# Kernel optimization log

Hardware: AMD Instinct MI355X
Metric: run time of the kernel (lower is better)

## Reference

```python
import jax, jax.numpy as jnp
import numpy as np

N_QUESTIONS = 2000
N_CATS = 4
MEMORY_SIZE = 50
KEY_DIM = 50
VALUE_DIM = 200
FINAL_FC = 50
ABILITY_SCALE = 3.0
BATCH = 1024
SEQ_LEN = 500


def setup_inputs() -> dict:
    key = jax.random.key(0)
    ks = jax.random.split(key, 20)
    f32 = jnp.float32
    inp = {}
    # integer data: question ids in [1, n_questions], responses in [0, K)
    inp['q_data'] = jax.random.randint(ks[0], (BATCH, SEQ_LEN), 1, N_QUESTIONS + 1)
    inp['r_data'] = jax.random.randint(ks[1], (BATCH, SEQ_LEN), 0, N_CATS)
    s = 0.05
    inp['q_embed_w'] = jax.random.normal(ks[2], (N_QUESTIONS + 1, KEY_DIM), f32) * s
    inp['Mk'] = jax.random.normal(ks[3], (MEMORY_SIZE, KEY_DIM), f32) * s
    inp['Mv0'] = jax.random.normal(ks[4], (MEMORY_SIZE, VALUE_DIM), f32) * s
    inp['Wv'] = jax.random.normal(ks[5], (VALUE_DIM, N_CATS * N_QUESTIONS), f32) * s
    inp['bv'] = jnp.zeros((VALUE_DIM,), f32)
    # DKVMN erase / add transforms
    inp['We'] = jax.random.normal(ks[6], (VALUE_DIM, VALUE_DIM), f32) * s
    inp['be'] = jnp.zeros((VALUE_DIM,), f32)
    inp['Wa'] = jax.random.normal(ks[7], (VALUE_DIM, VALUE_DIM), f32) * s
    inp['ba'] = jnp.zeros((VALUE_DIM,), f32)
    # summary network
    inp['Ws'] = jax.random.normal(ks[8], (FINAL_FC, VALUE_DIM + KEY_DIM), f32) * s
    inp['bs'] = jnp.zeros((FINAL_FC,), f32)
    # ability / threshold / discrimination heads
    inp['Wth'] = jax.random.normal(ks[9], (1, FINAL_FC), f32) * s
    inp['bth'] = jnp.zeros((1,), f32)
    inp['Wbeta'] = jax.random.normal(ks[10], (N_CATS - 1, KEY_DIM), f32) * s
    inp['bbeta'] = jnp.zeros((N_CATS - 1,), f32)
    inp['Wdisc'] = jax.random.normal(ks[11], (1, FINAL_FC + KEY_DIM), f32) * s
    inp['bdisc'] = jnp.zeros((1,), f32)
    return inp


def _deep_gpcm(q_data, r_data, q_embed_w, Mk, Mv0, Wv, bv, We, be, Wa, ba,
               Ws, bs, Wth, bth, Wbeta, bbeta, Wdisc, bdisc):
    B, S = q_data.shape
    K = Wbeta.shape[0] + 1
    D = Wv.shape[0]
    Q = Wv.shape[1] // K
    # view gpcm_value_embed weight as (D, K, Q): one-hot(q) @ W == gather column q
    WvK = Wv.reshape(D, K, Q)
    k_idx = jnp.arange(K, dtype=jnp.float32)
    Mv_init = jnp.broadcast_to(Mv0[None], (B,) + Mv0.shape)

    def step(Mv, inp):
        q_t, r_t = inp  # (B,), (B,)
        qe = q_embed_w[q_t]  # (B, key_dim)
        # linear decay weights: max(0, 1 - |k - r| / (K-1))
        w = jnp.maximum(0.0, 1.0 - jnp.abs(k_idx[None, :] - r_t[:, None].astype(jnp.float32)) / (K - 1))  # (B, K)
        Wvq = jnp.take(WvK, q_t - 1, axis=2)  # (D, K, B)
        ve = jnp.einsum('dkb,bk->bd', Wvq, w) + bv  # value embedding (B, D)
        # DKVMN attention + read
        cw = jax.nn.softmax(qe @ Mk.T, axis=-1)  # (B, mem)
        read = jnp.einsum('bm,bmd->bd', cw, Mv)
        # summary / IRT heads
        summary = jnp.tanh(jnp.concatenate([read, qe], axis=-1) @ Ws.T + bs)  # (B, fc)
        theta = ABILITY_SCALE * (summary @ Wth.T + bth)[:, 0]  # (B,)
        betas = jnp.tanh(qe @ Wbeta.T + bbeta)  # (B, K-1)
        alpha = jax.nn.softplus(jnp.concatenate([summary, qe], axis=-1) @ Wdisc.T + bdisc)[:, 0]  # (B,)
        # erase-add memory write
        erase = jax.nn.sigmoid(ve @ We.T + be)
        add = jnp.tanh(ve @ Wa.T + ba)
        Mv_new = Mv * (1.0 - cw[:, :, None] * erase[:, None, :]) + cw[:, :, None] * add[:, None, :]
        # GPCM cumulative logits -> softmax
        cum = jnp.cumsum(alpha[:, None] * (theta[:, None] - betas), axis=-1)  # (B, K-1)
        logits = jnp.concatenate([jnp.zeros((B, 1), cum.dtype), cum], axis=-1)  # (B, K)
        probs = jax.nn.softmax(logits, axis=-1)
        return Mv_new, probs

    _, probs = jax.lax.scan(step, Mv_init, (q_data.T, r_data.T))  # (S, B, K)
    return jnp.transpose(probs, (1, 0, 2))  # (B, S, K)


def reference(q_data, r_data, q_embed_w, Mk, Mv0, Wv, bv, We, be, Wa, ba,
              Ws, bs, Wth, bth, Wbeta, bbeta, Wdisc, bdisc):
    return _deep_gpcm(q_data, r_data, q_embed_w, Mk, Mv0, Wv, bv, We, be, Wa, ba,
                      Ws, bs, Wth, bth, Wbeta, bbeta, Wdisc, bdisc)
```

## Files before the change

kernel.cpp:

```cpp
#include <hip/hip_runtime.h>
#include <hip/hip_bf16.h>
#include <cstdint>
#include <cstddef>


namespace {
constexpr int kB   = 1024;
constexpr int kS   = 500;
constexpr int kQ   = 2000;
constexpr int kKD  = 50;
constexpr int kMem = 50;
constexpr int kD   = 200;
constexpr int kFC  = 50;
constexpr int kWP  = 216;

constexpr size_t OFF_EAD  = 0;
constexpr size_t OFF_CW   = OFF_EAD + (size_t)kQ * 4 * kD * 2;
constexpr size_t OFF_SQ   = OFF_CW + 100064;
constexpr size_t OFF_BQ   = OFF_SQ + 100064;
constexpr size_t OFF_DQ   = OFF_BQ + 8032;
constexpr size_t OFF_CE   = OFF_DQ + 2016;
constexpr size_t OFF_CA   = OFF_CE + 224;
constexpr size_t OFF_WET  = OFF_CA + 224;
constexpr size_t OFF_WAT  = OFF_WET + 40000;
}

typedef float f32x2 __attribute__((ext_vector_type(2)));
typedef _Float16 h2_t __attribute__((ext_vector_type(2)));

__device__ __forceinline__ f32x2 pk_fma(f32x2 a, f32x2 b, f32x2 c) {
  f32x2 d;
  asm("v_pk_fma_f32 %0, %1, %2, %3" : "=v"(d) : "v"(a), "v"(b), "v"(c));
  return d;
}

__device__ __forceinline__ void lds_barrier() {
  asm volatile("s_waitcnt lgkmcnt(0)" ::: "memory");
  __builtin_amdgcn_s_barrier();
  asm volatile("" ::: "memory");
}

__device__ __forceinline__ float fast_tanh(float x) {
  const float ax = fabsf(x);
  const float t = __expf(-2.f * ax);
  const float r = (1.f - t) / (1.f + t);
  return copysignf(r, x);
}
__device__ __forceinline__ float fast_softplus(float x) {
  return fmaxf(x, 0.f) + log1pf(__expf(-fabsf(x)));
}

__global__ void prep1_misc(const float* __restrict__ We, const float* __restrict__ Wa,
                           const float* __restrict__ bv, const float* __restrict__ be,
                           const float* __restrict__ ba, float* __restrict__ ws) {
  float* WeT = ws + OFF_WET;
  float* WaT = ws + OFF_WAT;
  float* ce  = ws + OFF_CE;
  float* ca  = ws + OFF_CA;
  const int gt = blockIdx.x * 256 + threadIdx.x;
  const int stride = gridDim.x * 256;
  for (int e = gt; e < kD * kD; e += stride) {
    const int i = e / kD;
    const int dd = e - i * kD;
    WeT[e] = We[dd * kD + i];
    WaT[e] = Wa[dd * kD + i];
  }
  for (int dd = gt; dd < kD; dd += stride) {
    float acc_e = be[dd], acc_a = ba[dd];
    for (int i = 0; i < kD; ++i) {
      acc_e = fmaf(We[dd * kD + i], bv[i], acc_e);
      acc_a = fmaf(Wa[dd * kD + i], bv[i], acc_a);
    }
    ce[dd] = acc_e;
    ca[dd] = acc_a;
  }
}

__global__ void prep2_ead(const float* __restrict__ Wv, float* __restrict__ ws) {
  __shared__ float s_wv[4][kD];
  const int tid = threadIdx.x;
  const int qm1 = blockIdx.x;
  for (int e = tid; e < 4 * kD; e += 256) {
    const int k = e / kD;
    const int i = e - k * kD;
    s_wv[k][i] = Wv[(size_t)i * (4 * kQ) + (size_t)k * kQ + qm1];
  }
  __syncthreads();
  const int d = tid;
  if (d < kD) {
    const float* WeT = ws + OFF_WET;
    const float* WaT = ws + OFF_WAT;
    float e0 = 0.f, e1 = 0.f, e2 = 0.f, e3 = 0.f;
    float a0 = 0.f, a1 = 0.f, a2 = 0.f, a3 = 0.f;
    for (int i = 0; i < kD; ++i) {
      const float we = WeT[i * kD + d];
      const float wa = WaT[i * kD + d];
      e0 = fmaf(we, s_wv[0][i], e0);
      e1 = fmaf(we, s_wv[1][i], e1);
      e2 = fmaf(we, s_wv[2][i], e2);
      e3 = fmaf(we, s_wv[3][i], e3);
      a0 = fmaf(wa, s_wv[0][i], a0);
      a1 = fmaf(wa, s_wv[1][i], a1);
      a2 = fmaf(wa, s_wv[2][i], a2);
      a3 = fmaf(wa, s_wv[3][i], a3);
    }
    const float ced = ws[OFF_CE + d];
    const float cad = ws[OFF_CA + d];
    const float W[4][4] = {{1.f, 2.f / 3.f, 1.f / 3.f, 0.f},
                           {2.f / 3.f, 1.f, 2.f / 3.f, 1.f / 3.f},
                           {1.f / 3.f, 2.f / 3.f, 1.f, 2.f / 3.f},
                           {0.f, 1.f / 3.f, 2.f / 3.f, 1.f}};
#pragma unroll
    for (int r = 0; r < 4; ++r) {
      const float ep = ced + W[r][0] * e0 + W[r][1] * e1 + W[r][2] * e2 + W[r][3] * e3;
      const float ap = cad + W[r][0] * a0 + W[r][1] * a1 + W[r][2] * a2 + W[r][3] * a3;
      float2 v;
      v.x = 1.f / (1.f + expf(-ep));
      v.y = tanhf(ap);
      *reinterpret_cast<float2*>(ws + OFF_EAD + ((size_t)(qm1 * 4 + r) * kD + d) * 2) = v;
    }
  }
}

__global__ void prep3_qtables(const float* __restrict__ q_embed_w, const float* __restrict__ Mk,
                              const float* __restrict__ Ws, const float* __restrict__ bs,
                              const float* __restrict__ Wbeta, const float* __restrict__ bbeta,
                              const float* __restrict__ Wdisc, float* __restrict__ ws) {
  __shared__ float s_qe[kKD];
  const int tid = threadIdx.x;
  const int q = blockIdx.x;
  if (tid < kKD) s_qe[tid] = q_embed_w[q * kKD + tid];
  __syncthreads();
  {
    float s = -1e30f;
    if (tid < kMem) {
      s = 0.f;
      for (int j = 0; j < kKD; ++j) s = fmaf(s_qe[j], Mk[tid * kKD + j], s);
    }
    float mx = s;
#pragma unroll
    for (int o = 1; o < 64; o <<= 1) mx = fmaxf(mx, __shfl_xor(mx, o));
    const float ev = (tid < kMem) ? expf(s - mx) : 0.f;
    float sm = ev;
#pragma unroll
    for (int o = 1; o < 64; o <<= 1) sm += __shfl_xor(sm, o);
    if (tid < kMem) ws[OFF_CW + (size_t)q * kMem + tid] = ev / sm;
  }
  if (tid < kFC) {
    float s = bs[tid];
    for (int j = 0; j < kKD; ++j) s = fmaf(s_qe[j], Ws[tid * 250 + kD + j], s);
    ws[OFF_SQ + (size_t)q * kFC + tid] = s;
  }
  if (tid < 4) {
    float v = 0.f;
    if (tid < 3) {
      float s = bbeta[tid];
      for (int j = 0; j < kKD; ++j) s = fmaf(s_qe[j], Wbeta[tid * kKD + j], s);
      v = tanhf(s);
    }
    ws[OFF_BQ + (size_t)q * 4 + tid] = v;
  }
  if (tid == 0) {
    float s = 0.f;
    for (int j = 0; j < kKD; ++j) s = fmaf(s_qe[j], Wdisc[kFC + j], s);
    ws[OFF_DQ + q] = s;
  }
}

__device__ __forceinline__ void do_finale(int l, float wth_f, float wds_f, float bth0,
                                          float bdisc0, const float (*s_part)[64],
                                          const float* s_sq_row, const float* s_bqdq_row,
                                          float* out_ptr) {
  float summ = 0.f;
  if (l < kFC) {
    const float sp = s_part[0][l] + s_part[1][l] + s_part[2][l] + s_part[3][l] +
                     s_part[4][l] + s_sq_row[l];
    summ = fast_tanh(sp);
  }
  float p1 = wth_f * summ;
  float p2 = wds_f * summ;
#pragma unroll
  for (int o = 1; o < 64; o <<= 1) {
    p1 += __shfl_xor(p1, o);
    p2 += __shfl_xor(p2, o);
  }
  if (l == 0) {
    const float theta = 3.f * (p1 + bth0);
    const float alpha = fast_softplus(p2 + s_bqdq_row[3] + bdisc0);
    const float c1 = alpha * (theta - s_bqdq_row[0]);
    const float c2 = c1 + alpha * (theta - s_bqdq_row[1]);
    const float c3 = c2 + alpha * (theta - s_bqdq_row[2]);
    const float mx = fmaxf(fmaxf(0.f, c1), fmaxf(c2, c3));
    const float x0 = __expf(0.f - mx);
    const float x1 = __expf(c1 - mx);
    const float x2 = __expf(c2 - mx);
    const float x3 = __expf(c3 - mx);
    const float inv = 1.f / (x0 + x1 + x2 + x3);
    float4 pr;
    pr.x = x0 * inv;
    pr.y = x1 * inv;
    pr.z = x2 * inv;
    pr.w = x3 * inv;
    *reinterpret_cast<float4*>(out_ptr) = pr;
  }
}

#define STEP(PB, I3, T, TN1, TN2)                                                     \
  {                                                                                   \
    constexpr int IP1_ = ((I3) + 1) % 3;                                              \
    f32x2 en2 = {0.f, 0.f}, ad2 = {0.f, 0.f};                                         \
    float2 ea_nxt = ea_cur;                                                           \
    if (dact) {                                                                       \
      ea_nxt = EAD2[(size_t)s_qr[(TN1)] * kD + d];                                    \
      en2[0] = -ea_cur.x;                                                             \
      en2[1] = -ea_cur.x;                                                             \
      ad2[0] = ea_cur.y;                                                              \
      ad2[1] = ea_cur.y;                                                              \
    }                                                                                 \
    if (wid == 0 && lane < kMem) {                 \
      s_cw[(PB) ^ 1][lane] = cw_cur;                                                  \
      cw_cur = CW[s_q[(TN2)] * kMem + lane];                                          \
    }                                                                                 \
    if (wid == 1) {         \
      const int qn_ = s_q[(TN1)];                                                     \
      if (lane < kFC) {                                                               \
        s_sq[(I3)][lane] = v2_cur;                                                    \
        v2_cur = SQ[qn_ * kFC + lane];                                                \
      } else if (lane < 53) {                                                         \
        s_bqdq[(I3)][lane - 50] = v2_cur;                                             \
        v2_cur = BQ[qn_ * 4 + (lane - 50)];                                           \
      } else if (lane == 53) {                                                        \
        s_bqdq[(I3)][3] = v2_cur;                                                     \
        v2_cur = DQ[qn_];                                                             \
      }                                                                               \
    }                                                                                 \
    if (dact) {                    \
      f32x2 r2a = {0.f, 0.f}, r2b = {0.f, 0.f};                                       \
      const float4* cw4_ = reinterpret_cast<const float4*>(s_cw[(PB)]);               \
      _Pragma("unroll") for (int g = 0; g < 12; ++g) {                                \
        const float4 c4_ = cw4_[g];                                                   \
        const f32x2 clo_ = {c4_.x, c4_.y};                                            \
        const f32x2 chi_ = {c4_.z, c4_.w};                                            \
        r2a = pk_fma(clo_, mv[2 * g], r2a);                                           \
        mv[2 * g] = pk_fma(clo_, pk_fma(mv[2 * g], en2, ad2), mv[2 * g]);             \
        r2b = pk_fma(chi_, mv[2 * g + 1], r2b);                                       \
        mv[2 * g + 1] = pk_fma(chi_, pk_fma(mv[2 * g + 1], en2, ad2), mv[2 * g + 1]); \
      }                                                                               \
      {                                                                               \
        const f32x2 cl_ = *reinterpret_cast<const f32x2*>(&s_cw[(PB)][48]);           \
        r2a = pk_fma(cl_, mv[24], r2a);                                               \
        mv[24] = pk_fma(cl_, pk_fma(mv[24], en2, ad2), mv[24]);                       \
      }                                                                               \
      s_readh[(PB)][d] = (_Float16)((r2a[0] + r2b[0]) + (r2a[1] + r2b[1]));           \
    }                                                                                 \
    if (wid == 0 && (T) >= 2) {                              \
      do_finale(lane, wth_f, wds_f, bth0, bdisc0, s_part[(PB) ^ 1], s_sq[IP1_],       \
                s_bqdq[IP1_], out_b + (size_t)((T) - 2) * 4);                         \
    }                                                                                 \
    if (tid < 250) {                    \
      const float4* wp_ = reinterpret_cast<const float4*>(s_wsh + pf * kWP + pc * 40);\
      const float4* rp_ = reinterpret_cast<const float4*>(&s_readh[(PB) ^ 1][pc * 40]);\
      float a0_ = 0.f, a1_ = 0.f;                                                     \
      _Pragma("unroll") for (int g = 0; g < 5; ++g) {                                 \
        const float4 wv_ = wp_[g];                                                    \
        const float4 rv_ = rp_[g];                                                    \
        a0_ = __builtin_amdgcn_fdot2(__builtin_bit_cast(h2_t, wv_.x),                 \
                                     __builtin_bit_cast(h2_t, rv_.x), a0_, false);    \
        a1_ = __builtin_amdgcn_fdot2(__builtin_bit_cast(h2_t, wv_.y),                 \
                                     __builtin_bit_cast(h2_t, rv_.y), a1_, false);    \
        a0_ = __builtin_amdgcn_fdot2(__builtin_bit_cast(h2_t, wv_.z),                 \
                                     __builtin_bit_cast(h2_t, rv_.z), a0_, false);    \
        a1_ = __builtin_amdgcn_fdot2(__builtin_bit_cast(h2_t, wv_.w),                 \
                                     __builtin_bit_cast(h2_t, rv_.w), a1_, false);    \
      }                                                                               \
      s_part[(PB)][pc][pf] = a0_ + a1_;                                               \
    }                                                                                 \
    lds_barrier();                                       \
    ea_cur = ea_nxt;                                                                  \
  }

__launch_bounds__(256, 4)
__global__ void dkvmn_main(const int* __restrict__ q_data, const int* __restrict__ r_data,
                           const float* __restrict__ Mv0, const float* __restrict__ Ws,
                           const float* __restrict__ Wth, const float* __restrict__ bth,
                           const float* __restrict__ Wdisc, const float* __restrict__ bdisc,
                           const float* __restrict__ ws, float* __restrict__ out) {
  const int tid = threadIdx.x;
  const int b = blockIdx.x;
  const int lane = tid & 63;
  const int wid = tid >> 6;
  const float2* EAD2 = reinterpret_cast<const float2*>(ws + OFF_EAD);
  const float* CW = ws + OFF_CW;
  const float* SQ = ws + OFF_SQ;
  const float* BQ = ws + OFF_BQ;
  const float* DQ = ws + OFF_DQ;

  __shared__ __align__(16) _Float16 s_wsh[kFC * kWP];
  __shared__ __align__(16) _Float16 s_readh[2][208];
  __shared__ __align__(16) float s_cw[2][64];
  __shared__ float s_part[2][5][64];
  __shared__ float s_sq[3][52];
  __shared__ float s_bqdq[3][4];
  __shared__ int s_q[kS];
  __shared__ int s_qr[kS];

  for (int e = tid; e < kFC * kD; e += 256) {
    const int f = e / kD;
    const int dd = e - f * kD;
    s_wsh[f * kWP + dd] = (_Float16)Ws[f * 250 + dd];
  }
  {
    const int* qrow = q_data + (size_t)b * kS;
    const int* rrow = r_data + (size_t)b * kS;
    for (int e = tid; e < kS; e += 256) {
      const int qv = qrow[e];
      s_q[e] = qv;
      s_qr[e] = (qv - 1) * 4 + rrow[e];
    }
  }
  const int d = tid;
  const bool dact = (d < kD);
  const int pc = tid / 50;
  const int pf = tid - pc * 50;
  f32x2 mv[25];
#pragma unroll
  for (int m = 0; m < 25; ++m) mv[m] = f32x2{0.f, 0.f};
  if (dact) {
#pragma unroll
    for (int m = 0; m < 25; ++m) {
      mv[m][0] = Mv0[(2 * m) * kD + d];
      mv[m][1] = Mv0[(2 * m + 1) * kD + d];
    }
  }
  float wth_f = 0.f, wds_f = 0.f;
  if (wid == 0 && lane < kFC) {
    wth_f = Wth[lane];
    wds_f = Wdisc[lane];
  }
  const float bth0 = bth[0];
  const float bdisc0 = bdisc[0];
  float* out_b = out + (size_t)b * kS * 4;
  __syncthreads();

  const int q0 = s_q[0];
  const int q1 = s_q[1];
  float2 ea_cur = make_float2(0.f, 0.f);
  if (dact) ea_cur = EAD2[(size_t)s_qr[0] * kD + d];
  float cw_cur = 0.f;
  if (wid == 0 && lane < kMem) {
    s_cw[0][lane] = CW[q0 * kMem + lane];
    cw_cur = CW[q1 * kMem + lane];
  }
  float v2_cur = 0.f;
  if (wid == 1) {
    if (lane < kFC) v2_cur = SQ[q0 * kFC + lane];
    else if (lane < 53) v2_cur = BQ[q0 * 4 + (lane - 50)];
    else if (lane == 53) v2_cur = DQ[q0];
  }
  __syncthreads();

  for (int it = 0; it < 83; ++it) {
    const int t0 = 6 * it;
    STEP(0, 0, t0 + 0, t0 + 1, t0 + 2)
    STEP(1, 1, t0 + 1, t0 + 2, t0 + 3)
    STEP(0, 2, t0 + 2, t0 + 3, t0 + 4)
    STEP(1, 0, t0 + 3, t0 + 4, t0 + 5)
    STEP(0, 1, t0 + 4, t0 + 5, t0 + 6)
    STEP(1, 2, t0 + 5, t0 + 6, t0 + 7)
  }
  STEP(0, 0, 498, 499, 499)
  STEP(1, 1, 499, 499, 499)

  {
    constexpr int pbE = kS & 1;
    constexpr int i3a = (kS - 2) % 3;
    constexpr int i3b = (kS - 1) % 3;
    if (tid < 250) {
      const float4* wp = reinterpret_cast<const float4*>(s_wsh + pf * kWP + pc * 40);
      const float4* rp = reinterpret_cast<const float4*>(&s_readh[(kS - 1) & 1][pc * 40]);
      float acc0 = 0.f, acc1 = 0.f;
#pragma unroll
      for (int g = 0; g < 5; ++g) {
        const float4 wv = wp[g];
        const float4 rv = rp[g];
        acc0 = __builtin_amdgcn_fdot2(__builtin_bit_cast(h2_t, wv.x),
                                      __builtin_bit_cast(h2_t, rv.x), acc0, false);
        acc1 = __builtin_amdgcn_fdot2(__builtin_bit_cast(h2_t, wv.y),
                                      __builtin_bit_cast(h2_t, rv.y), acc1, false);
        acc0 = __builtin_amdgcn_fdot2(__builtin_bit_cast(h2_t, wv.z),
                                      __builtin_bit_cast(h2_t, rv.z), acc0, false);
        acc1 = __builtin_amdgcn_fdot2(__builtin_bit_cast(h2_t, wv.w),
                                      __builtin_bit_cast(h2_t, rv.w), acc1, false);
      }
      s_part[pbE][pc][pf] = acc0 + acc1;
    }
    if (wid == 0) {
      do_finale(lane, wth_f, wds_f, bth0, bdisc0, s_part[pbE ^ 1], s_sq[i3a], s_bqdq[i3a],
                out_b + (size_t)(kS - 2) * 4);
    }
    lds_barrier();
    if (wid == 0) {
      do_finale(lane, wth_f, wds_f, bth0, bdisc0, s_part[pbE], s_sq[i3b], s_bqdq[i3b],
                out_b + (size_t)(kS - 1) * 4);
    }
  }
}

extern "C" void kernel_launch(void* const* d_in, const int* in_sizes, int n_in,
                              void* d_out, int out_size, void* d_ws, size_t ws_size,
                              hipStream_t stream) {
  (void)in_sizes; (void)n_in; (void)out_size; (void)ws_size;
  const int* q_data = (const int*)d_in[0];
  const int* r_data = (const int*)d_in[1];
  const float* q_embed_w = (const float*)d_in[2];
  const float* Mk = (const float*)d_in[3];
  const float* Mv0 = (const float*)d_in[4];
  const float* Wv = (const float*)d_in[5];
  const float* bv = (const float*)d_in[6];
  const float* We = (const float*)d_in[7];
  const float* be = (const float*)d_in[8];
  const float* Wa = (const float*)d_in[9];
  const float* ba = (const float*)d_in[10];
  const float* Ws = (const float*)d_in[11];
  const float* bs = (const float*)d_in[12];
  const float* Wth = (const float*)d_in[13];
  const float* bth = (const float*)d_in[14];
  const float* Wbeta = (const float*)d_in[15];
  const float* bbeta = (const float*)d_in[16];
  const float* Wdisc = (const float*)d_in[17];
  const float* bdisc = (const float*)d_in[18];
  float* out = (float*)d_out;
  float* ws = (float*)d_ws;

  hipLaunchKernelGGL(prep1_misc, dim3(64), dim3(256), 0, stream, We, Wa, bv, be, ba, ws);
  hipLaunchKernelGGL(prep2_ead, dim3(kQ), dim3(256), 0, stream, Wv, ws);
  hipLaunchKernelGGL(prep3_qtables, dim3(kQ + 1), dim3(64), 0, stream, q_embed_w, Mk, Ws, bs,
                     Wbeta, bbeta, Wdisc, ws);
  hipLaunchKernelGGL(dkvmn_main, dim3(kB), dim3(256), 0, stream, q_data, r_data, Mv0, Ws, Wth,
                     bth, Wdisc, bdisc, ws, out);
}
```

Baseline: 1.266 ms.

## Split recurrence and summary head into separate kernels via fp16 read buffer

The fused per-step kernel is split in two. A recurrence kernel updates memory and writes each step's fp16 read vector to a global workspace buffer, taking two barriers per four steps with cw double-buffered ahead. A head kernel then streams those reads and runs the summary dot products and GPCM softmax. This takes the head work and most barriers off the serial critical path, at the cost of writing and reading about 200 MB of intermediates; it only runs when the workspace is large enough and otherwise falls back to the fused kernel.

```diff
diff --git a/kernel.cpp b/kernel.cpp
--- a/kernel.cpp
+++ b/kernel.cpp
@@ -23,6 +23,8 @@
 constexpr size_t OFF_CA   = OFF_CE + 224;
 constexpr size_t OFF_WET  = OFF_CA + 224;
 constexpr size_t OFF_WAT  = OFF_WET + 40000;
+constexpr size_t OFF_R    = 3490816;
+constexpr size_t NEED_WS  = OFF_R * 4 + (size_t)kB * kS * kD * 2;
 }
 
 typedef float f32x2 __attribute__((ext_vector_type(2)));
@@ -205,6 +207,223 @@
   }
 }
 
+#define RSTEP(BR, BW, T, EAC, CWW)                                                    \
+  {                                                                                   \
+    f32x2 en2 = {0.f, 0.f}, ad2 = {0.f, 0.f};                                         \
+    if (dact) {                                                                       \
+      en2[0] = -EAC.x; en2[1] = -EAC.x;                                               \
+      ad2[0] = EAC.y;  ad2[1] = EAC.y;                                                \
+      EAC = EAD2[(size_t)s_qr[(T) + 2] * kD + d];               \
+    }                                                                                 \
+    if (cwact) {                                                                      \
+      s_cw[BW][cj] = CWW;                                       \
+      CWW = CW[s_q[(T) + 4] * kMem + cj];                       \
+    }                                                                                 \
+    if (dact) {                                                                       \
+      f32x2 r2a = {0.f, 0.f}, r2b = {0.f, 0.f};                                       \
+      const float4* cw4_ = reinterpret_cast<const float4*>(s_cw[BR]);                 \
+      _Pragma("unroll") for (int g = 0; g < 12; ++g) {                                \
+        const float4 c4_ = cw4_[g];                                                   \
+        const f32x2 clo_ = {c4_.x, c4_.y};                                            \
+        const f32x2 chi_ = {c4_.z, c4_.w};                                            \
+        r2a = pk_fma(clo_, mv[2 * g], r2a);                                           \
+        mv[2 * g] = pk_fma(clo_, pk_fma(mv[2 * g], en2, ad2), mv[2 * g]);             \
+        r2b = pk_fma(chi_, mv[2 * g + 1], r2b);                                       \
+        mv[2 * g + 1] = pk_fma(chi_, pk_fma(mv[2 * g + 1], en2, ad2), mv[2 * g + 1]); \
+      }                                                                               \
+      {                                                                               \
+        const f32x2 cl_ = *reinterpret_cast<const f32x2*>(&s_cw[BR][48]);             \
+        r2a = pk_fma(cl_, mv[24], r2a);                                               \
+        mv[24] = pk_fma(cl_, pk_fma(mv[24], en2, ad2), mv[24]);                       \
+      }                                                                               \
+      Rb[(size_t)(T) * kD + d] = (_Float16)((r2a[0] + r2b[0]) + (r2a[1] + r2b[1]));   \
+    }                                                                                 \
+  }
+
+__launch_bounds__(256, 4)
+__global__ void dkvmn_rec(const int* __restrict__ q_data, const int* __restrict__ r_data,
+                          const float* __restrict__ Mv0, const float* __restrict__ ws,
+                          _Float16* __restrict__ R) {
+  const int tid = threadIdx.x;
+  const int b = blockIdx.x;
+  const float2* EAD2 = reinterpret_cast<const float2*>(ws + OFF_EAD);
+  const float* CW = ws + OFF_CW;
+
+  __shared__ __align__(16) float s_cw[4][64];
+  __shared__ int s_q[504];
+  __shared__ int s_qr[504];
+
+  {
+    const int* qrow = q_data + (size_t)b * kS;
+    const int* rrow = r_data + (size_t)b * kS;
+    for (int e = tid; e < kS; e += 256) {
+      const int qv = qrow[e];
+      s_q[e] = qv;
+      s_qr[e] = (qv - 1) * 4 + rrow[e];
+    }
+  }
+  const int d = tid;
+  const bool dact = (d < kD);
+  const bool cwact = (tid >= 200 && tid < 250);
+  const int cj = tid - 200;
+  f32x2 mv[25];
+#pragma unroll
+  for (int m = 0; m < 25; ++m) mv[m] = f32x2{0.f, 0.f};
+  if (dact) {
+#pragma unroll
+    for (int m = 0; m < 25; ++m) {
+      mv[m][0] = Mv0[(2 * m) * kD + d];
+      mv[m][1] = Mv0[(2 * m + 1) * kD + d];
+    }
+  }
+  _Float16* Rb = R + (size_t)b * kS * kD;
+  __syncthreads();
+  if (tid < 4) {
+    s_q[500 + tid] = s_q[499];
+    s_qr[500 + tid] = s_qr[499];
+  }
+  float cwE = 0.f, cwO = 0.f;
+  if (cwact) {
+    s_cw[0][cj] = CW[s_q[0] * kMem + cj];
+    s_cw[1][cj] = CW[s_q[1] * kMem + cj];
+    cwE = CW[s_q[2] * kMem + cj];
+    cwO = CW[s_q[3] * kMem + cj];
+  }
+  float2 eaE = make_float2(0.f, 0.f), eaO = eaE;
+  if (dact) {
+    eaE = EAD2[(size_t)s_qr[0] * kD + d];
+    eaO = EAD2[(size_t)s_qr[1] * kD + d];
+  }
+  __syncthreads();
+
+  for (int jt = 0; jt < 125; ++jt) {
+    const int t0 = 4 * jt;
+    RSTEP(0, 2, t0 + 0, eaE, cwE)
+    RSTEP(1, 3, t0 + 1, eaO, cwO)
+    lds_barrier();
+    RSTEP(2, 0, t0 + 2, eaE, cwE)
+    RSTEP(3, 1, t0 + 3, eaO, cwO)
+    lds_barrier();
+  }
+}
+
+__launch_bounds__(256, 4)
+__global__ void dkvmn_head(const int* __restrict__ q_data, const _Float16* __restrict__ R,
+                           const float* __restrict__ Ws, const float* __restrict__ Wth,
+                           const float* __restrict__ bth, const float* __restrict__ Wdisc,
+                           const float* __restrict__ bdisc, const float* __restrict__ ws,
+                           float* __restrict__ out) {
+  const int tid = threadIdx.x;
+  const int b = blockIdx.x;
+  const int lane = tid & 63;
+  const int wid = tid >> 6;
+  const float* SQ = ws + OFF_SQ;
+  const float* BQ = ws + OFF_BQ;
+  const float* DQ = ws + OFF_DQ;
+
+  __shared__ __align__(16) _Float16 s_wsh[kFC * kWP];
+  __shared__ __align__(16) _Float16 s_readh[2][208];
+  __shared__ float s_part[2][5][64];
+  __shared__ float s_sq[3][52];
+  __shared__ float s_bqdq[3][4];
+  __shared__ int s_q[kS];
+
+  for (int e = tid; e < kFC * kD; e += 256) {
+    const int f = e / kD;
+    const int dd = e - f * kD;
+    s_wsh[f * kWP + dd] = (_Float16)Ws[f * 250 + dd];
+  }
+  {
+    const int* qrow = q_data + (size_t)b * kS;
+    for (int e = tid; e < kS; e += 256) s_q[e] = qrow[e];
+  }
+  const int pc = tid / 50;
+  const int pf = tid - pc * 50;
+  const bool ract = (tid >= 128 && tid < 228);
+  const int ru = tid - 128;
+  float wth_f = 0.f, wds_f = 0.f;
+  if (wid == 0 && lane < kFC) {
+    wth_f = Wth[lane];
+    wds_f = Wdisc[lane];
+  }
+  const float bth0 = bth[0];
+  const float bdisc0 = bdisc[0];
+  const _Float16* Rb = R + (size_t)b * kS * kD;
+  float* out_b = out + (size_t)b * kS * 4;
+  __syncthreads();
+
+  unsigned int rv_cur = 0;
+  if (ract) {
+    *reinterpret_cast<unsigned int*>(&s_readh[0][2 * ru]) =
+        reinterpret_cast<const unsigned int*>(Rb)[ru];
+    rv_cur = reinterpret_cast<const unsigned int*>(Rb + kD)[ru];
+  }
+  float v2_cur = 0.f;
+  if (wid == 1) {
+    const int q0 = s_q[0];
+    if (lane < kFC) s_sq[0][lane] = SQ[q0 * kFC + lane];
+    else if (lane < 53) s_bqdq[0][lane - 50] = BQ[q0 * 4 + (lane - 50)];
+    else if (lane == 53) s_bqdq[0][3] = DQ[q0];
+    const int q1 = s_q[1];
+    if (lane < kFC) v2_cur = SQ[q1 * kFC + lane];
+    else if (lane < 53) v2_cur = BQ[q1 * 4 + (lane - 50)];
+    else if (lane == 53) v2_cur = DQ[q1];
+  }
+  __syncthreads();
+
+  for (int t = 0; t < kS; ++t) {
+    const int pb = t & 1;
+    if (ract) {
+      *reinterpret_cast<unsigned int*>(&s_readh[pb ^ 1][2 * ru]) = rv_cur;
+      const int t2 = (t + 2 < kS) ? t + 2 : kS - 1;
+      rv_cur = reinterpret_cast<const unsigned int*>(Rb + (size_t)t2 * kD)[ru];
+    }
+    if (wid == 1) {
+      const int i3n = (t + 1) % 3;
+      const int qn = s_q[(t + 2 < kS) ? t + 2 : kS - 1];
+      if (lane < kFC) {
+        s_sq[i3n][lane] = v2_cur;
+        v2_cur = SQ[qn * kFC + lane];
+      } else if (lane < 53) {
+        s_bqdq[i3n][lane - 50] = v2_cur;
+        v2_cur = BQ[qn * 4 + (lane - 50)];
+      } else if (lane == 53) {
+        s_bqdq[i3n][3] = v2_cur;
+        v2_cur = DQ[qn];
+      }
+    }
+    if (tid < 250) {
+      const float4* wp = reinterpret_cast<const float4*>(s_wsh + pf * kWP + pc * 40);
+      const float4* rp = reinterpret_cast<const float4*>(&s_readh[pb][pc * 40]);
+      float acc0 = 0.f, acc1 = 0.f;
+#pragma unroll
+      for (int g = 0; g < 5; ++g) {
+        const float4 wv = wp[g];
+        const float4 rv = rp[g];
+        acc0 = __builtin_amdgcn_fdot2(__builtin_bit_cast(h2_t, wv.x),
+                                      __builtin_bit_cast(h2_t, rv.x), acc0, false);
+        acc1 = __builtin_amdgcn_fdot2(__builtin_bit_cast(h2_t, wv.y),
+                                      __builtin_bit_cast(h2_t, rv.y), acc1, false);
+        acc0 = __builtin_amdgcn_fdot2(__builtin_bit_cast(h2_t, wv.z),
+                                      __builtin_bit_cast(h2_t, rv.z), acc0, false);
+        acc1 = __builtin_amdgcn_fdot2(__builtin_bit_cast(h2_t, wv.w),
+                                      __builtin_bit_cast(h2_t, rv.w), acc1, false);
+      }
+      s_part[pb][pc][pf] = acc0 + acc1;
+    }
+    if (wid == 0 && t >= 1) {
+      const int i3p = (t - 1) % 3;
+      do_finale(lane, wth_f, wds_f, bth0, bdisc0, s_part[pb ^ 1], s_sq[i3p], s_bqdq[i3p],
+                out_b + (size_t)(t - 1) * 4);
+    }
+    lds_barrier();
+  }
+  if (wid == 0) {
+    do_finale(lane, wth_f, wds_f, bth0, bdisc0, s_part[(kS - 1) & 1], s_sq[(kS - 1) % 3],
+              s_bqdq[(kS - 1) % 3], out_b + (size_t)(kS - 1) * 4);
+  }
+}
+
 #define STEP(PB, I3, T, TN1, TN2)                                                     \
   {                                                                                   \
     constexpr int IP1_ = ((I3) + 1) % 3;                                              \
@@ -217,11 +436,11 @@
       ad2[0] = ea_cur.y;                                                              \
       ad2[1] = ea_cur.y;                                                              \
     }                                                                                 \
-    if (wid == 0 && lane < kMem) {                 \
+    if (wid == 0 && lane < kMem) {                                                    \
       s_cw[(PB) ^ 1][lane] = cw_cur;                                                  \
       cw_cur = CW[s_q[(TN2)] * kMem + lane];                                          \
     }                                                                                 \
-    if (wid == 1) {         \
+    if (wid == 1) {                                                                   \
       const int qn_ = s_q[(TN1)];                                                     \
       if (lane < kFC) {                                                               \
         s_sq[(I3)][lane] = v2_cur;                                                    \
@@ -234,7 +453,7 @@
         v2_cur = DQ[qn_];                                                             \
       }                                                                               \
     }                                                                                 \
-    if (dact) {                    \
+    if (dact) {                                                                       \
       f32x2 r2a = {0.f, 0.f}, r2b = {0.f, 0.f};                                       \
       const float4* cw4_ = reinterpret_cast<const float4*>(s_cw[(PB)]);               \
       _Pragma("unroll") for (int g = 0; g < 12; ++g) {                                \
@@ -253,11 +472,11 @@
       }                                                                               \
       s_readh[(PB)][d] = (_Float16)((r2a[0] + r2b[0]) + (r2a[1] + r2b[1]));           \
     }                                                                                 \
-    if (wid == 0 && (T) >= 2) {                              \
+    if (wid == 0 && (T) >= 2) {                                                       \
       do_finale(lane, wth_f, wds_f, bth0, bdisc0, s_part[(PB) ^ 1], s_sq[IP1_],       \
                 s_bqdq[IP1_], out_b + (size_t)((T) - 2) * 4);                         \
     }                                                                                 \
-    if (tid < 250) {                    \
+    if (tid < 250) {                                                                  \
       const float4* wp_ = reinterpret_cast<const float4*>(s_wsh + pf * kWP + pc * 40);\
       const float4* rp_ = reinterpret_cast<const float4*>(&s_readh[(PB) ^ 1][pc * 40]);\
       float a0_ = 0.f, a1_ = 0.f;                                                     \
@@ -275,7 +494,7 @@
       }                                                                               \
       s_part[(PB)][pc][pf] = a0_ + a1_;                                               \
     }                                                                                 \
-    lds_barrier();                                       \
+    lds_barrier();                                                                    \
     ea_cur = ea_nxt;                                                                  \
   }
 
@@ -409,7 +628,7 @@
 extern "C" void kernel_launch(void* const* d_in, const int* in_sizes, int n_in,
                               void* d_out, int out_size, void* d_ws, size_t ws_size,
                               hipStream_t stream) {
-  (void)in_sizes; (void)n_in; (void)out_size; (void)ws_size;
+  (void)in_sizes; (void)n_in; (void)out_size;
   const int* q_data = (const int*)d_in[0];
   const int* r_data = (const int*)d_in[1];
   const float* q_embed_w = (const float*)d_in[2];
@@ -436,6 +655,13 @@
   hipLaunchKernelGGL(prep2_ead, dim3(kQ), dim3(256), 0, stream, Wv, ws);
   hipLaunchKernelGGL(prep3_qtables, dim3(kQ + 1), dim3(64), 0, stream, q_embed_w, Mk, Ws, bs,
                      Wbeta, bbeta, Wdisc, ws);
-  hipLaunchKernelGGL(dkvmn_main, dim3(kB), dim3(256), 0, stream, q_data, r_data, Mv0, Ws, Wth,
-                     bth, Wdisc, bdisc, ws, out);
-}
+  if (ws_size >= NEED_WS) {
+    _Float16* R = reinterpret_cast<_Float16*>(ws + OFF_R);
+    hipLaunchKernelGGL(dkvmn_rec, dim3(kB), dim3(256), 0, stream, q_data, r_data, Mv0, ws, R);
+    hipLaunchKernelGGL(dkvmn_head, dim3(kB), dim3(256), 0, stream, q_data, R, Ws, Wth, bth,
+                       Wdisc, bdisc, ws, out);
+  } else {
+    hipLaunchKernelGGL(dkvmn_main, dim3(kB), dim3(256), 0, stream, q_data, r_data, Mv0, Ws, Wth,
+                       bth, Wdisc, bdisc, ws, out);
+  }
+}
```

After: 1.119 ms. 11.6% less time.
